# Kernel optimization log

Hardware: AMD Instinct MI355X
Metric: run time of the kernel (lower is better)

## Reference

```python
import jax, jax.numpy as jnp
import numpy as np

B = 65536
T = 512
DT = 0.01  # time-grid spacing


def setup_inputs() -> dict:
    key = jax.random.key(0)
    k1, k2 = jax.random.split(key)
    y0 = jax.random.normal(k1, (B, 3), dtype=jnp.float32)
    t_span = jnp.arange(T, dtype=jnp.float32) * DT
    params = jax.random.uniform(k2, (B, 3), dtype=jnp.float32)
    return {"y0": y0, "t_span": t_span, "params": params}


def _bloch_rhs_incomplete(y, params):
    # y: [B,3] -> (u, v, w); params: [B,3] -> Omega = params[:,0], gamma = params[:,2]
    u = y[:, 0:1]
    v = y[:, 1:2]
    w = y[:, 2:3]
    Omega = params[:, 0:1]
    gamma = params[:, 2:3]
    du = -gamma * u
    dv = -gamma * v - Omega * w
    dw = -2.0 * gamma * (w + 1.0) + Omega * v
    return jnp.concatenate([du, dv, dw], axis=-1)


def reference(y0, t_span, params):
    dts = t_span[1:] - t_span[:-1]  # [T-1]

    def rk4_step(y, dt):
        k1 = _bloch_rhs_incomplete(y, params)
        k2 = _bloch_rhs_incomplete(y + 0.5 * dt * k1, params)
        k3 = _bloch_rhs_incomplete(y + 0.5 * dt * k2, params)
        k4 = _bloch_rhs_incomplete(y + dt * k3, params)
        y_new = y + dt / 6.0 * (k1 + 2.0 * k2 + 2.0 * k3 + k4)
        return y_new, y_new

    _, ys = jax.lax.scan(rk4_step, y0, dts)  # ys: [T-1, B, 3]
    return jnp.concatenate([y0[None], ys], axis=0)  # [T, B, 3]
```

## Files before the change

kernel.cpp:

```cpp
#include <hip/hip_runtime.h>


#define NB 65536
#define NT 512

__global__ __launch_bounds__(256) void bloch_rk4_kernel(
    const float* __restrict__ y0,
    const float* __restrict__ tspan,
    const float* __restrict__ params,
    float* __restrict__ out)
{
    __shared__ float sdt[NT];
    const int tid = threadIdx.x;
    for (int i = tid; i < NT; i += 256) {
        float d = 0.0f;
        if (i < NT - 1) d = tspan[i + 1] - tspan[i];
        sdt[i] = d;
    }
    __syncthreads();

    const int b   = blockIdx.x * 256 + tid;
    const int ib3 = b * 3;

    float u = y0[ib3 + 0];
    float v = y0[ib3 + 1];
    float w = y0[ib3 + 2];
    const float Om = params[ib3 + 0];
    const float g  = params[ib3 + 2];
    const float g2 = 2.0f * g;

    out[ib3 + 0] = u;
    out[ib3 + 1] = v;
    out[ib3 + 2] = w;

    float dt = sdt[0];
    for (int i = 1; i < NT; ++i) {
        const float dt_next = sdt[i];

        const float k1u = -g * u;
        const float k1v = -g * v - Om * w;
        const float k1w = Om * v - g2 * w - g2;

        const float h = 0.5f * dt;
        float uu = u + h * k1u;
        float vv = v + h * k1v;
        float ww = w + h * k1w;

        const float k2u = -g * uu;
        const float k2v = -g * vv - Om * ww;
        const float k2w = Om * vv - g2 * ww - g2;

        uu = u + h * k2u;
        vv = v + h * k2v;
        ww = w + h * k2w;

        const float k3u = -g * uu;
        const float k3v = -g * vv - Om * ww;
        const float k3w = Om * vv - g2 * ww - g2;

        uu = u + dt * k3u;
        vv = v + dt * k3v;
        ww = w + dt * k3w;

        const float k4u = -g * uu;
        const float k4v = -g * vv - Om * ww;
        const float k4w = Om * vv - g2 * ww - g2;

        const float s = dt * (1.0f / 6.0f);
        u += s * (k1u + 2.0f * k2u + 2.0f * k3u + k4u);
        v += s * (k1v + 2.0f * k2v + 2.0f * k3v + k4v);
        w += s * (k1w + 2.0f * k2w + 2.0f * k3w + k4w);

        const size_t o = (size_t)i * (NB * 3) + (size_t)ib3;
        out[o + 0] = u;
        out[o + 1] = v;
        out[o + 2] = w;

        dt = dt_next;
    }
}

extern "C" void kernel_launch(void* const* d_in, const int* in_sizes, int n_in,
                              void* d_out, int out_size, void* d_ws, size_t ws_size,
                              hipStream_t stream) {
    const float* y0     = (const float*)d_in[0];
    const float* tspan  = (const float*)d_in[1];
    const float* params = (const float*)d_in[2];
    float* out = (float*)d_out;

    bloch_rk4_kernel<<<NB / 256, 256, 0, stream>>>(y0, tspan, params, out);
}
```

Baseline: 403.6 us.

## Split RK4 integration into checkpoint pass and parallel chunk-refill pass

The serial time loop is split into two kernels. The first integrates every trajectory and stores the state only at chunk boundaries, every 32 steps. The second launches one block per (batch group, chunk) and recomputes each chunk from its stored checkpoint, writing the full output. This exposes far more parallelism than the original 256 blocks and spreads the output writes over many more waves, at the cost of roughly doubling the arithmetic and adding a second launch.

Measured after the change: 463.1 us. +14.8%, slower.

```diff
diff --git a/kernel.cpp b/kernel.cpp
--- a/kernel.cpp
+++ b/kernel.cpp
@@ -3,8 +3,50 @@
 
 #define NB 65536
 #define NT 512
+#define CHUNK 32
+#define NCH (NT / CHUNK)
+#define NB3 (NB * 3)
 
-__global__ __launch_bounds__(256) void bloch_rk4_kernel(
+__device__ __forceinline__ void rk4_step(
+    float& u, float& v, float& w,
+    const float Om, const float g, const float g2, const float dt)
+{
+    const float k1u = -g * u;
+    const float k1v = -g * v - Om * w;
+    const float k1w = Om * v - g2 * w - g2;
+
+    const float h = 0.5f * dt;
+    float uu = u + h * k1u;
+    float vv = v + h * k1v;
+    float ww = w + h * k1w;
+
+    const float k2u = -g * uu;
+    const float k2v = -g * vv - Om * ww;
+    const float k2w = Om * vv - g2 * ww - g2;
+
+    uu = u + h * k2u;
+    vv = v + h * k2v;
+    ww = w + h * k2w;
+
+    const float k3u = -g * uu;
+    const float k3v = -g * vv - Om * ww;
+    const float k3w = Om * vv - g2 * ww - g2;
+
+    uu = u + dt * k3u;
+    vv = v + dt * k3v;
+    ww = w + dt * k3w;
+
+    const float k4u = -g * uu;
+    const float k4v = -g * vv - Om * ww;
+    const float k4w = Om * vv - g2 * ww - g2;
+
+    const float s = dt * (1.0f / 6.0f);
+    u += s * (k1u + 2.0f * k2u + 2.0f * k3u + k4u);
+    v += s * (k1v + 2.0f * k2v + 2.0f * k3v + k4v);
+    w += s * (k1w + 2.0f * k2w + 2.0f * k3w + k4w);
+}
+
+__global__ __launch_bounds__(256) void bloch_phaseA(
     const float* __restrict__ y0,
     const float* __restrict__ tspan,
     const float* __restrict__ params,
@@ -34,49 +76,62 @@
     out[ib3 + 2] = w;
 
     float dt = sdt[0];
-    for (int i = 1; i < NT; ++i) {
-        const float dt_next = sdt[i];
-
-        const float k1u = -g * u;
-        const float k1v = -g * v - Om * w;
-        const float k1w = Om * v - g2 * w - g2;
-
-        const float h = 0.5f * dt;
-        float uu = u + h * k1u;
-        float vv = v + h * k1v;
-        float ww = w + h * k1w;
-
-        const float k2u = -g * uu;
-        const float k2v = -g * vv - Om * ww;
-        const float k2w = Om * vv - g2 * ww - g2;
-
-        uu = u + h * k2u;
-        vv = v + h * k2v;
-        ww = w + h * k2w;
-
-        const float k3u = -g * uu;
-        const float k3v = -g * vv - Om * ww;
-        const float k3w = Om * vv - g2 * ww - g2;
-
-        uu = u + dt * k3u;
-        vv = v + dt * k3v;
-        ww = w + dt * k3w;
-
-        const float k4u = -g * uu;
-        const float k4v = -g * vv - Om * ww;
-        const float k4w = Om * vv - g2 * ww - g2;
-
-        const float s = dt * (1.0f / 6.0f);
-        u += s * (k1u + 2.0f * k2u + 2.0f * k3u + k4u);
-        v += s * (k1v + 2.0f * k2v + 2.0f * k3v + k4v);
-        w += s * (k1w + 2.0f * k2w + 2.0f * k3w + k4w);
-
-        const size_t o = (size_t)i * (NB * 3) + (size_t)ib3;
+    for (int j = 1; j < NCH; ++j) {
+        const int ibase = (j - 1) * CHUNK;
+#pragma unroll
+        for (int k = 0; k < CHUNK; ++k) {
+            const float dtn = sdt[ibase + k + 1];
+            rk4_step(u, v, w, Om, g, g2, dt);
+            dt = dtn;
+        }
+        const size_t o = (size_t)(j * CHUNK) * NB3 + (size_t)ib3;
         out[o + 0] = u;
         out[o + 1] = v;
         out[o + 2] = w;
+    }
+}
 
-        dt = dt_next;
+__global__ __launch_bounds__(256) void bloch_phaseB(
+    const float* __restrict__ tspan,
+    const float* __restrict__ params,
+    float* __restrict__ out)
+{
+    __shared__ float sdt[CHUNK];
+    const int tid = threadIdx.x;
+    const int bx  = blockIdx.x;
+    const int j   = bx & (NCH - 1);
+    const int sg  = bx >> 4;
+    const int i0  = j * CHUNK;
+
+    if (tid < CHUNK) {
+        const int idx = i0 + tid;
+        float d = 0.0f;
+        if (idx + 1 < NT) d = tspan[idx + 1] - tspan[idx];
+        sdt[tid] = d;
+    }
+    __syncthreads();
+
+    const int b   = sg * 256 + tid;
+    const int ib3 = b * 3;
+    const float Om = params[ib3 + 0];
+    const float g  = params[ib3 + 2];
+    const float g2 = 2.0f * g;
+
+    size_t o = (size_t)i0 * NB3 + (size_t)ib3;
+    float u = out[o + 0];
+    float v = out[o + 1];
+    float w = out[o + 2];
+
+    float dt = sdt[0];
+#pragma unroll 4
+    for (int k = 0; k < CHUNK - 1; ++k) {
+        const float dtn = sdt[k + 1];
+        rk4_step(u, v, w, Om, g, g2, dt);
+        o += NB3;
+        out[o + 0] = u;
+        out[o + 1] = v;
+        out[o + 2] = w;
+        dt = dtn;
     }
 }
 
@@ -88,5 +143,6 @@
     const float* params = (const float*)d_in[2];
     float* out = (float*)d_out;
 
-    bloch_rk4_kernel<<<NB / 256, 256, 0, stream>>>(y0, tspan, params, out);
+    bloch_phaseA<<<NB / 256, 256, 0, stream>>>(y0, tspan, params, out);
+    bloch_phaseB<<<(NB / 256) * NCH, 256, 0, stream>>>(tspan, params, out);
 }
```
